# Kernel tuning notes

Hardware: AMD Instinct MI355X
Metric: run time of the kernel (lower is better)

The kernel has to match this reference:

```python
import jax, jax.numpy as jnp
import numpy as np

IN_C, HID1, HID2 = 128, 256, 32
N_NODES = 50000
N_EDGES = 1600000
N_LABEL = 200000


def setup_inputs() -> dict:
    key = jax.random.key(0)
    ks = jax.random.split(key, 8)
    x = jax.random.normal(ks[0], (N_NODES, IN_C), dtype=jnp.float32)
    edge_index = jax.random.randint(ks[1], (2, N_EDGES), 0, N_NODES, dtype=jnp.int64)
    edge_label_index = jax.random.randint(ks[2], (2, N_LABEL), 0, N_NODES, dtype=jnp.int64)
    # GCNConv params (glorot-ish scale), bias zeros as default init
    W1 = jax.random.normal(ks[3], (IN_C, HID1), dtype=jnp.float32) * (1.0 / np.sqrt(IN_C))
    b1 = jnp.zeros((HID1,), dtype=jnp.float32)
    W2 = jax.random.normal(ks[4], (HID1, HID2), dtype=jnp.float32) * (1.0 / np.sqrt(HID1))
    b2 = jnp.zeros((HID2,), dtype=jnp.float32)
    return {"x": x, "edge_index": edge_index, "edge_label_index": edge_label_index,
            "W1": W1, "b1": b1, "W2": W2, "b2": b2}


def _gcn_conv(x, W, b, src, dst, n_nodes):
    # GCNConv: h = x @ W; add self-loops; symmetric deg^{-1/2} normalization; scatter-add; + bias
    h = x @ W  # [N, out]
    loop = jnp.arange(n_nodes, dtype=src.dtype)
    s = jnp.concatenate([src, loop])
    d = jnp.concatenate([dst, loop])
    deg = jax.ops.segment_sum(jnp.ones_like(d, dtype=h.dtype), d, num_segments=n_nodes)
    dinv = jnp.where(deg > 0, jax.lax.rsqrt(deg), 0.0)
    coef = dinv[s] * dinv[d]  # [E+N]
    msg = h[s] * coef[:, None]  # irregular gather, [E+N, out]
    agg = jax.ops.segment_sum(msg, d, num_segments=n_nodes)
    return agg + b


def reference(x, edge_index, edge_label_index, W1, b1, W2, b2):
    n = x.shape[0]
    src, dst = edge_index[0], edge_index[1]
    # encode (dropout p=0, use_bn=False -> identity)
    h = _gcn_conv(x, W1, b1, src, dst, n)
    h = jax.nn.relu(h)
    z = _gcn_conv(h, W2, b2, src, dst, n)
    # decode: edge-wise dot product
    return (z[edge_label_index[0]] * z[edge_label_index[1]]).sum(axis=-1)
```

## Files before the change

kernel.cpp:

```cpp
#include <hip/hip_runtime.h>
#include <hip/hip_fp16.h>

#define IN_C 128
#define H1   256
#define H2   32
#define BWL  6
#define NBMAX 1024
#define BCAP 2560
#define CSRCAP 4096

typedef _Float16 half8 __attribute__((ext_vector_type(8)));
typedef _Float16 half4 __attribute__((ext_vector_type(4)));
typedef _Float16 h2    __attribute__((ext_vector_type(2)));
typedef float f32x4 __attribute__((ext_vector_type(4)));
typedef unsigned short us8 __attribute__((ext_vector_type(8)));
typedef unsigned short us4 __attribute__((ext_vector_type(4)));

__global__ __launch_bounds__(256) void k_scatter(const int* __restrict__ src, const int* __restrict__ dst,
                                                 int* bucket_cursor, unsigned int* __restrict__ binned,
                                                 const float* __restrict__ W1, const float* __restrict__ W2,
                                                 _Float16* __restrict__ W1s, _Float16* __restrict__ W2s,
                                                 int e, int nb) {
  __shared__ int hist[NBMAX];
  __shared__ int wbase[NBMAX];
  int t = threadIdx.x;
  for (int u = t; u < nb; u += 256) hist[u] = 0;
  __syncthreads();
  int base = blockIdx.x * 8192;
  int s_[32], d_[32], r_[32];
  #pragma unroll
  for (int j = 0; j < 32; j++) {
    int i = base + j * 256 + t;
    if (i < e) {
      s_[j] = src[i]; d_[j] = dst[i];
      r_[j] = atomicAdd(&hist[d_[j] >> BWL], 1);
    } else d_[j] = -1;
  }
  __syncthreads();
  for (int u = t; u < nb; u += 256) {
    int c = hist[u];
    wbase[u] = (c > 0) ? (u * BCAP + atomicAdd(&bucket_cursor[u], c)) : 0;
  }
  __syncthreads();
  #pragma unroll
  for (int j = 0; j < 32; j++) {
    if (d_[j] >= 0)
      binned[wbase[d_[j] >> BWL] + r_[j]] = ((unsigned)(d_[j] & 63) << 16) | (unsigned)s_[j];
  }
  int i = blockIdx.x * 256 + t;
  if (i < 128 * 256) {
    int d = i >> 3, j = i & 7;
    int mrow = d & 15, quad = (d >> 4) & 3, ks = (d >> 6) & 3, nt = d >> 8;
    W1s[i] = (_Float16)W1[(ks * 32 + quad * 8 + j) * 256 + nt * 16 + mrow];
  }
  if (i < 32 * 256) {
    int d = i >> 3, j = i & 7;
    int mrow = d & 15, quad = (d >> 4) & 3, ks = (d >> 6) & 7, nt = d >> 9;
    W2s[i] = (_Float16)W2[(ks * 32 + quad * 8 + j) * 32 + nt * 16 + mrow];
  }
}

__global__ __launch_bounds__(256) void k_fill2(const unsigned int* __restrict__ binned,
                                               const int* __restrict__ bucket_cursor,
                                               unsigned short* __restrict__ csr16,
                                               int* __restrict__ offsets, int* __restrict__ ecnt,
                                               float* __restrict__ dinv,
                                               const float4* __restrict__ x4, half4* __restrict__ xh4,
                                               int n, int nb) {
  __shared__ int cnt[64], pre[64], loc[64];
  __shared__ float sdinv[64];
  int b = blockIdx.x;
  int t = threadIdx.x;
  if (t < 64) cnt[t] = 0;
  {
    us8 dv;
    #pragma unroll
    for (int q = 0; q < 8; q++) dv[q] = (unsigned short)n;
    us8* cp = (us8*)(csr16 + (size_t)b * CSRCAP);
    for (int i = t; i < CSRCAP / 8; i += 256) cp[i] = dv;
  }
  __syncthreads();
  int start = b * BCAP, end = start + bucket_cursor[b];
  int startc = b * CSRCAP;
  int node0 = b << BWL;
  unsigned int recs[10]; int ranks[10];
  int ne = 0;
  for (int i = start + t; i < end; i += 256) {
    unsigned int rec = binned[i];
    int li = (int)(rec >> 16);
    ranks[ne] = atomicAdd(&cnt[li], 1);
    recs[ne++] = rec;
  }
  __syncthreads();
  int v = (t < 64) ? cnt[t] : 0;
  int vp = (v + 31) & ~31;
  if (t < 64) pre[t] = vp;
  __syncthreads();
  for (int off = 1; off < 64; off <<= 1) {
    int x = (t >= off && t < 64) ? pre[t - off] : 0;
    __syncthreads();
    if (t < 64) pre[t] += x;
    __syncthreads();
  }
  if (t < 64) {
    int excl = pre[t] - vp;
    loc[t] = excl;
    float dn = rsqrtf((float)(v + 1));
    sdinv[t] = dn;
    int node = node0 + t;
    if (node < n) {
      offsets[node] = startc + excl;
      ecnt[node] = v;
      dinv[node] = dn;
    }
  }
  __syncthreads();
  for (int k = 0; k < ne; k++) {
    int li = (int)(recs[k] >> 16);
    csr16[startc + loc[li] + ranks[k]] = (unsigned short)(recs[k] & 0xFFFFu);
  }
  for (int q = t; q < 64 * 32; q += 256) {
    int nd = node0 + (q >> 5);
    if (nd < n) {
      int c4 = q & 31;
      float4 vv = x4[(size_t)nd * 32 + c4];
      float dn = sdinv[q >> 5];
      half4 o;
      o[0] = (_Float16)(vv.x * dn); o[1] = (_Float16)(vv.y * dn);
      o[2] = (_Float16)(vv.z * dn); o[3] = (_Float16)(vv.w * dn);
      xh4[(size_t)nd * 32 + c4] = o;
    }
  }
}

__global__ __launch_bounds__(256) void k_agg1(const half8* __restrict__ xh8, const float* __restrict__ dinv,
                                              const int* __restrict__ ecnt, const int* __restrict__ offsets,
                                              const unsigned short* __restrict__ csr16,
                                              half8* __restrict__ aggh8, int n) {
  int node = blockIdx.x * 4 + (threadIdx.x >> 6);
  int lane = threadIdx.x & 63;
  int g = lane >> 4;
  int c8 = lane & 15;
  if (node >= n) return;
  float acc[8];
  #pragma unroll
  for (int k = 0; k < 8; k++) acc[k] = 0.f;
  int start = offsets[node];
  int cnt = ecnt[node];
  int units = ((cnt + 31) & ~31) >> 5;
  us8 idx = *(const us8*)(csr16 + start + g * 8);
  for (int u = 0; u < units; u++) {
    half8 v0 = xh8[(size_t)idx[0] * 16 + c8], v1 = xh8[(size_t)idx[1] * 16 + c8];
    half8 v2 = xh8[(size_t)idx[2] * 16 + c8], v3 = xh8[(size_t)idx[3] * 16 + c8];
    half8 v4 = xh8[(size_t)idx[4] * 16 + c8], v5 = xh8[(size_t)idx[5] * 16 + c8];
    half8 v6 = xh8[(size_t)idx[6] * 16 + c8], v7 = xh8[(size_t)idx[7] * 16 + c8];
    us8 nidx = *(const us8*)(csr16 + start + ((u + 1) << 5) + g * 8);
    asm volatile("" :: "v"(v0), "v"(v1), "v"(v2), "v"(v3), "v"(v4), "v"(v5), "v"(v6), "v"(v7));
    half8 s = (((v0 + v1) + (v2 + v3)) + ((v4 + v5) + (v6 + v7)));
    #pragma unroll
    for (int k = 0; k < 8; k++) acc[k] += (float)s[k];
    idx = nidx;
  }
  #pragma unroll
  for (int k = 0; k < 8; k++) {
    acc[k] += __shfl_xor(acc[k], 16, 64);
    acc[k] += __shfl_xor(acc[k], 32, 64);
  }
  if (g == 0) {
    half8 selfv = xh8[(size_t)node * 16 + c8];
    float dn = dinv[node];
    half8 o;
    #pragma unroll
    for (int k = 0; k < 8; k++) o[k] = (_Float16)((acc[k] + (float)selfv[k]) * dn);
    aggh8[(size_t)node * 16 + c8] = o;
  }
}

__global__ __launch_bounds__(256) void k_gemm12(const _Float16* __restrict__ aggh,
                                                const _Float16* __restrict__ W1s, const float* __restrict__ b1,
                                                const _Float16* __restrict__ W2s, const float* __restrict__ dinv,
                                                _Float16* __restrict__ h2h, int n) {
  __shared__ _Float16 wlds[128 * 256];
  int wid = threadIdx.x >> 6, lane = threadIdx.x & 63;
  int quad = lane >> 4, mrow = lane & 15;
  int mbase = blockIdx.x * 64 + wid * 16;
  int node = mbase + mrow; if (node >= n) node = n - 1;
  {
    half8* wl8 = (half8*)wlds;
    const half8* wg8 = (const half8*)W1s;
    for (int i = threadIdx.x; i < 4096; i += 256) wl8[i] = wg8[i];
  }
  __syncthreads();
  const half8* A = (const half8*)aggh;
  const half8* BL = (const half8*)wlds;
  f32x4 acc[16];
  #pragma unroll
  for (int t = 0; t < 16; t++) acc[t] = (f32x4){0.f, 0.f, 0.f, 0.f};
  half8 a_cur = A[(size_t)node * 16 + quad];
  #pragma unroll
  for (int ks = 0; ks < 4; ks++) {
    half8 a = a_cur;
    if (ks < 3) a_cur = A[(size_t)node * 16 + (ks + 1) * 4 + quad];
    #pragma unroll
    for (int nt = 0; nt < 16; nt++) {
      half8 b = BL[(nt * 4 + ks) * 64 + lane];
      acc[nt] = __builtin_amdgcn_mfma_f32_16x16x32_f16(a, b, acc[nt], 0, 0, 0);
    }
  }
  __syncthreads();
  _Float16* h1t = wlds;
  #pragma unroll
  for (int nt = 0; nt < 16; nt++) {
    int c = nt * 16 + mrow;
    float bias = b1[c];
    #pragma unroll
    for (int r = 0; r < 4; r++)
      h1t[(wid * 16 + quad * 4 + r) * 264 + c] = (_Float16)fmaxf(acc[nt][r] + bias, 0.f);
  }
  __syncthreads();
  const half8* B2 = (const half8*)W2s;
  f32x4 acc2[2];
  acc2[0] = (f32x4){0.f, 0.f, 0.f, 0.f};
  acc2[1] = (f32x4){0.f, 0.f, 0.f, 0.f};
  #pragma unroll
  for (int ks = 0; ks < 8; ks++) {
    const half8* arow = (const half8*)&h1t[(wid * 16 + mrow) * 264 + ks * 32 + quad * 8];
    half8 a = *arow;
    half8 b0 = B2[(0 * 8 + ks) * 64 + lane];
    half8 b1f = B2[(1 * 8 + ks) * 64 + lane];
    acc2[0] = __builtin_amdgcn_mfma_f32_16x16x32_f16(a, b0,  acc2[0], 0, 0, 0);
    acc2[1] = __builtin_amdgcn_mfma_f32_16x16x32_f16(a, b1f, acc2[1], 0, 0, 0);
  }
  #pragma unroll
  for (int nt = 0; nt < 2; nt++) {
    int c = nt * 16 + mrow;
    #pragma unroll
    for (int r = 0; r < 4; r++) {
      int m = mbase + quad * 4 + r;
      if (m < n) h2h[(size_t)m * H2 + c] = (_Float16)(acc2[nt][r] * dinv[m]);
    }
  }
}

__global__ __launch_bounds__(256) void k_agg2(const half4* __restrict__ h2h4, const float* __restrict__ dinv,
                                              const int* __restrict__ ecnt, const int* __restrict__ offsets,
                                              const unsigned short* __restrict__ csr16,
                                              const float* __restrict__ b2, half4* __restrict__ zh4, int n) {
  int node = blockIdx.x * 4 + (threadIdx.x >> 6);
  int lane = threadIdx.x & 63;
  int g = lane >> 3;
  int c4 = lane & 7;
  if (node >= n) return;
  float acc[4];
  #pragma unroll
  for (int k = 0; k < 4; k++) acc[k] = 0.f;
  int start = offsets[node];
  int cnt = ecnt[node];
  int units = ((cnt + 31) & ~31) >> 5;
  us4 idx = *(const us4*)(csr16 + start + g * 4);
  for (int u = 0; u < units; u++) {
    half4 vA = h2h4[(size_t)idx[0] * 8 + c4], vB = h2h4[(size_t)idx[1] * 8 + c4];
    half4 vC = h2h4[(size_t)idx[2] * 8 + c4], vD = h2h4[(size_t)idx[3] * 8 + c4];
    us4 nidx = *(const us4*)(csr16 + start + ((u + 1) << 5) + g * 4);
    asm volatile("" :: "v"(vA), "v"(vB), "v"(vC), "v"(vD));
    half4 sS = (vA + vB) + (vC + vD);
    #pragma unroll
    for (int k = 0; k < 4; k++) acc[k] += (float)sS[k];
    idx = nidx;
  }
  #pragma unroll
  for (int k = 0; k < 4; k++) {
    acc[k] += __shfl_xor(acc[k], 8, 64);
    acc[k] += __shfl_xor(acc[k], 16, 64);
    acc[k] += __shfl_xor(acc[k], 32, 64);
  }
  if (g == 0) {
    half4 selfv = h2h4[(size_t)node * 8 + c4];
    float dn = dinv[node];
    half4 o;
    #pragma unroll
    for (int k = 0; k < 4; k++) o[k] = (_Float16)((acc[k] + (float)selfv[k]) * dn + b2[c4 * 4 + k]);
    zh4[(size_t)node * 8 + c4] = o;
  }
}

__global__ __launch_bounds__(512) void k_decode(const half4* __restrict__ zh4, const int* __restrict__ eli,
                                                float* __restrict__ out, int L) {
  int p = blockIdx.x * 64 + (threadIdx.x >> 3);
  int c4 = threadIdx.x & 7;
  if (p >= L) return;
  int a = eli[p], b = eli[L + p];
  half4 za = zh4[(size_t)a * 8 + c4];
  half4 zb = zh4[(size_t)b * 8 + c4];
  h2 zal = {za[0], za[1]}, zah = {za[2], za[3]};
  h2 zbl = {zb[0], zb[1]}, zbh = {zb[2], zb[3]};
  float v = __builtin_amdgcn_fdot2(zal, zbl, __builtin_amdgcn_fdot2(zah, zbh, 0.f, false), false);
  #pragma unroll
  for (int off = 4; off >= 1; off >>= 1) v += __shfl_xor(v, off, 64);
  if (c4 == 0) out[p] = v;
}

extern "C" void kernel_launch(void* const* d_in, const int* in_sizes, int n_in,
                              void* d_out, int out_size, void* d_ws, size_t ws_size,
                              hipStream_t stream) {
  const float* x   = (const float*)d_in[0];
  const int*   ei  = (const int*)d_in[1];
  const int*   eli = (const int*)d_in[2];
  const float* W1  = (const float*)d_in[3];
  const float* b1  = (const float*)d_in[4];
  const float* W2  = (const float*)d_in[5];
  const float* b2  = (const float*)d_in[6];
  float* out = (float*)d_out;

  const int N = in_sizes[0] / IN_C;
  const int E = in_sizes[1] / 2;
  const int L = in_sizes[2] / 2;
  const int* e_src = ei;
  const int* e_dst = ei + E;
  const int NB = (N + 63) >> BWL;

  char* p = (char*)d_ws;
  auto carve = [&](size_t bytes) -> void* {
    void* r = (void*)p;
    p += (bytes + 255) & ~(size_t)255;
    return r;
  };
  int*   ecnt      = (int*)  carve((size_t)N * 4);
  float* dinv      = (float*)carve((size_t)N * 4);
  int*   offsets   = (int*)  carve((size_t)N * 4);
  int*   bcursor   = (int*)  carve((NBMAX + 1) * 4);
  _Float16* W1s    = (_Float16*)carve(256 * 128 * 2);
  _Float16* W2s    = (_Float16*)carve(32 * 256 * 2);
  unsigned short* csr16 = (unsigned short*)carve(((size_t)NB * CSRCAP + 64) * 2);
  unsigned int* binned  = (unsigned int*)carve((size_t)NB * BCAP * 4);
  h2*    xh        = (h2*)   carve((size_t)(N + 1) * IN_C * 2);
  h2*    aggh      = (h2*)   carve(((size_t)N + 64) * IN_C * 2);
  _Float16* h2h    = (_Float16*)carve(((size_t)N + 64) * H2 * 2);
  half4* zh4       = (half4*)carve((size_t)N * H2 * 2);
  half4* h2h4 = (half4*)h2h;

  const int B = 256;
  hipMemsetAsync(bcursor, 0, (size_t)(NBMAX + 1) * 4, stream);
  hipMemsetAsync((char*)xh + (size_t)N * IN_C * 2, 0, IN_C * 2, stream);
  hipMemsetAsync((char*)h2h + (size_t)N * H2 * 2, 0, H2 * 2, stream);
  k_scatter<<<(E + 8191) / 8192, B, 0, stream>>>(e_src, e_dst, bcursor, binned,
                                                 W1, W2, W1s, W2s, E, NB);
  k_fill2<<<NB, B, 0, stream>>>(binned, bcursor, csr16, offsets, ecnt, dinv,
                                (const float4*)x, (half4*)xh, N, NB);
  k_agg1<<<(N + 3) / 4, B, 0, stream>>>((const half8*)xh, dinv, ecnt, offsets, csr16, (half8*)aggh, N);
  k_gemm12<<<(N + 63) / 64, B, 0, stream>>>((const _Float16*)aggh, W1s, b1, W2s, dinv, h2h, N);
  k_agg2<<<(N + 3) / 4, B, 0, stream>>>(h2h4, dinv, ecnt, offsets, csr16, b2, zh4, N);
  k_decode<<<(L + 63) / 64, 512, 0, stream>>>(zh4, eli, out, L);
}
```

Measured before the change: 222.8 us.

## Pad CSR rows to 8 and restructure aggregation loops; fold dummy-row memsets into scatter

```diff
diff --git a/kernel.cpp b/kernel.cpp
--- a/kernel.cpp
+++ b/kernel.cpp
@@ -14,16 +14,20 @@
 typedef _Float16 h2    __attribute__((ext_vector_type(2)));
 typedef float f32x4 __attribute__((ext_vector_type(4)));
 typedef unsigned short us8 __attribute__((ext_vector_type(8)));
-typedef unsigned short us4 __attribute__((ext_vector_type(4)));
 
 __global__ __launch_bounds__(256) void k_scatter(const int* __restrict__ src, const int* __restrict__ dst,
                                                  int* bucket_cursor, unsigned int* __restrict__ binned,
                                                  const float* __restrict__ W1, const float* __restrict__ W2,
                                                  _Float16* __restrict__ W1s, _Float16* __restrict__ W2s,
+                                                 float* __restrict__ xh_dummy, float* __restrict__ h2h_dummy,
                                                  int e, int nb) {
   __shared__ int hist[NBMAX];
   __shared__ int wbase[NBMAX];
   int t = threadIdx.x;
+  if (blockIdx.x == 0) {
+    if (t < 64) xh_dummy[t] = 0.f;
+    if (t >= 64 && t < 80) h2h_dummy[t - 64] = 0.f;
+  }
   for (int u = t; u < nb; u += 256) hist[u] = 0;
   __syncthreads();
   int base = blockIdx.x * 8192;
@@ -93,7 +97,7 @@
   }
   __syncthreads();
   int v = (t < 64) ? cnt[t] : 0;
-  int vp = (v + 31) & ~31;
+  int vp = (v + 7) & ~7;
   if (t < 64) pre[t] = vp;
   __syncthreads();
   for (int off = 1; off < 64; off <<= 1) {
@@ -147,19 +151,17 @@
   for (int k = 0; k < 8; k++) acc[k] = 0.f;
   int start = offsets[node];
   int cnt = ecnt[node];
-  int units = ((cnt + 31) & ~31) >> 5;
-  us8 idx = *(const us8*)(csr16 + start + g * 8);
-  for (int u = 0; u < units; u++) {
-    half8 v0 = xh8[(size_t)idx[0] * 16 + c8], v1 = xh8[(size_t)idx[1] * 16 + c8];
-    half8 v2 = xh8[(size_t)idx[2] * 16 + c8], v3 = xh8[(size_t)idx[3] * 16 + c8];
-    half8 v4 = xh8[(size_t)idx[4] * 16 + c8], v5 = xh8[(size_t)idx[5] * 16 + c8];
-    half8 v6 = xh8[(size_t)idx[6] * 16 + c8], v7 = xh8[(size_t)idx[7] * 16 + c8];
-    us8 nidx = *(const us8*)(csr16 + start + ((u + 1) << 5) + g * 8);
-    asm volatile("" :: "v"(v0), "v"(v1), "v"(v2), "v"(v3), "v"(v4), "v"(v5), "v"(v6), "v"(v7));
-    half8 s = (((v0 + v1) + (v2 + v3)) + ((v4 + v5) + (v6 + v7)));
+  int qs = (cnt + 7) >> 3;
+  us8 id = *(const us8*)(csr16 + start);
+  for (int q = 0; q < qs; q++) {
+    int i0 = id[g], i1 = id[4 + g];
+    half8 v0 = xh8[(size_t)i0 * 16 + c8];
+    half8 v1 = xh8[(size_t)i1 * 16 + c8];
+    us8 nid = *(const us8*)(csr16 + start + (q + 1) * 8);
+    half8 s = v0 + v1;
     #pragma unroll
     for (int k = 0; k < 8; k++) acc[k] += (float)s[k];
-    idx = nidx;
+    id = nid;
   }
   #pragma unroll
   for (int k = 0; k < 8; k++) {
@@ -256,17 +258,22 @@
   for (int k = 0; k < 4; k++) acc[k] = 0.f;
   int start = offsets[node];
   int cnt = ecnt[node];
-  int units = ((cnt + 31) & ~31) >> 5;
-  us4 idx = *(const us4*)(csr16 + start + g * 4);
-  for (int u = 0; u < units; u++) {
-    half4 vA = h2h4[(size_t)idx[0] * 8 + c4], vB = h2h4[(size_t)idx[1] * 8 + c4];
-    half4 vC = h2h4[(size_t)idx[2] * 8 + c4], vD = h2h4[(size_t)idx[3] * 8 + c4];
-    us4 nidx = *(const us4*)(csr16 + start + ((u + 1) << 5) + g * 4);
-    asm volatile("" :: "v"(vA), "v"(vB), "v"(vC), "v"(vD));
-    half4 sS = (vA + vB) + (vC + vD);
-    #pragma unroll
-    for (int k = 0; k < 4; k++) acc[k] += (float)sS[k];
-    idx = nidx;
+  int qs = (cnt + 7) >> 3;
+  us8 id = *(const us8*)(csr16 + start);
+  for (int q = 0; q < qs; q += 2) {
+    us8 id2 = *(const us8*)(csr16 + start + (q + 1) * 8);
+    half4 v0 = h2h4[(size_t)(int)id[g] * 8 + c4];
+    half4 s;
+    if (q + 1 < qs) {
+      half4 v1 = h2h4[(size_t)(int)id2[g] * 8 + c4];
+      s = v0 + v1;
+    } else {
+      s = v0;
+    }
+    us8 nid = *(const us8*)(csr16 + start + (q + 2) * 8);
+    #pragma unroll
+    for (int k = 0; k < 4; k++) acc[k] += (float)s[k];
+    id = nid;
   }
   #pragma unroll
   for (int k = 0; k < 4; k++) {
@@ -341,10 +348,11 @@
 
   const int B = 256;
   hipMemsetAsync(bcursor, 0, (size_t)(NBMAX + 1) * 4, stream);
-  hipMemsetAsync((char*)xh + (size_t)N * IN_C * 2, 0, IN_C * 2, stream);
-  hipMemsetAsync((char*)h2h + (size_t)N * H2 * 2, 0, H2 * 2, stream);
   k_scatter<<<(E + 8191) / 8192, B, 0, stream>>>(e_src, e_dst, bcursor, binned,
-                                                 W1, W2, W1s, W2s, E, NB);
+                                                 W1, W2, W1s, W2s,
+                                                 (float*)((char*)xh + (size_t)N * IN_C * 2),
+                                                 (float*)((char*)h2h + (size_t)N * H2 * 2),
+                                                 E, NB);
   k_fill2<<<NB, B, 0, stream>>>(binned, bcursor, csr16, offsets, ecnt, dinv,
                                 (const float4*)x, (half4*)xh, N, NB);
   k_agg1<<<(N + 3) / 4, B, 0, stream>>>((const half8*)xh, dinv, ecnt, offsets, csr16, (half8*)aggh, N);
```

New measurement: 227.5 us. 2.1% more time.

## Replace two-pass bucketed CSR build with fixed-stride per-node atomic adjacency

Applied to the files above, without the earlier changes.

```diff
diff --git a/kernel.cpp b/kernel.cpp
--- a/kernel.cpp
+++ b/kernel.cpp
@@ -4,10 +4,7 @@
 #define IN_C 128
 #define H1   256
 #define H2   32
-#define BWL  6
-#define NBMAX 1024
-#define BCAP 2560
-#define CSRCAP 4096
+#define CSTRIDE 128
 
 typedef _Float16 half8 __attribute__((ext_vector_type(8)));
 typedef _Float16 half4 __attribute__((ext_vector_type(4)));
@@ -17,35 +14,25 @@
 typedef unsigned short us4 __attribute__((ext_vector_type(4)));
 
 __global__ __launch_bounds__(256) void k_scatter(const int* __restrict__ src, const int* __restrict__ dst,
-                                                 int* bucket_cursor, unsigned int* __restrict__ binned,
+                                                 int* __restrict__ ecnt, unsigned short* __restrict__ csr16,
                                                  const float* __restrict__ W1, const float* __restrict__ W2,
                                                  _Float16* __restrict__ W1s, _Float16* __restrict__ W2s,
-                                                 int e, int nb) {
-  __shared__ int hist[NBMAX];
-  __shared__ int wbase[NBMAX];
+                                                 float* __restrict__ xh_dummy, float* __restrict__ h2h_dummy,
+                                                 int e) {
   int t = threadIdx.x;
-  for (int u = t; u < nb; u += 256) hist[u] = 0;
-  __syncthreads();
+  if (blockIdx.x == 0) {
+    if (t < 64) xh_dummy[t] = 0.f;
+    if (t >= 64 && t < 80) h2h_dummy[t - 64] = 0.f;
+  }
   int base = blockIdx.x * 8192;
-  int s_[32], d_[32], r_[32];
   #pragma unroll
   for (int j = 0; j < 32; j++) {
     int i = base + j * 256 + t;
     if (i < e) {
-      s_[j] = src[i]; d_[j] = dst[i];
-      r_[j] = atomicAdd(&hist[d_[j] >> BWL], 1);
-    } else d_[j] = -1;
-  }
-  __syncthreads();
-  for (int u = t; u < nb; u += 256) {
-    int c = hist[u];
-    wbase[u] = (c > 0) ? (u * BCAP + atomicAdd(&bucket_cursor[u], c)) : 0;
-  }
-  __syncthreads();
-  #pragma unroll
-  for (int j = 0; j < 32; j++) {
-    if (d_[j] >= 0)
-      binned[wbase[d_[j] >> BWL] + r_[j]] = ((unsigned)(d_[j] & 63) << 16) | (unsigned)s_[j];
+      int s = src[i], d = dst[i];
+      int r = atomicAdd(&ecnt[d], 1);
+      csr16[(size_t)d * CSTRIDE + r] = (unsigned short)s;
+    }
   }
   int i = blockIdx.x * 256 + t;
   if (i < 128 * 256) {
@@ -60,65 +47,27 @@
   }
 }
 
-__global__ __launch_bounds__(256) void k_fill2(const unsigned int* __restrict__ binned,
-                                               const int* __restrict__ bucket_cursor,
-                                               unsigned short* __restrict__ csr16,
-                                               int* __restrict__ offsets, int* __restrict__ ecnt,
-                                               float* __restrict__ dinv,
-                                               const float4* __restrict__ x4, half4* __restrict__ xh4,
-                                               int n, int nb) {
-  __shared__ int cnt[64], pre[64], loc[64];
+__global__ __launch_bounds__(256) void k_fill(const int* __restrict__ ecnt, float* __restrict__ dinv,
+                                              unsigned short* __restrict__ csr16,
+                                              const float4* __restrict__ x4, half4* __restrict__ xh4,
+                                              int n) {
   __shared__ float sdinv[64];
   int b = blockIdx.x;
   int t = threadIdx.x;
-  if (t < 64) cnt[t] = 0;
-  {
-    us8 dv;
-    #pragma unroll
-    for (int q = 0; q < 8; q++) dv[q] = (unsigned short)n;
-    us8* cp = (us8*)(csr16 + (size_t)b * CSRCAP);
-    for (int i = t; i < CSRCAP / 8; i += 256) cp[i] = dv;
-  }
-  __syncthreads();
-  int start = b * BCAP, end = start + bucket_cursor[b];
-  int startc = b * CSRCAP;
-  int node0 = b << BWL;
-  unsigned int recs[10]; int ranks[10];
-  int ne = 0;
-  for (int i = start + t; i < end; i += 256) {
-    unsigned int rec = binned[i];
-    int li = (int)(rec >> 16);
-    ranks[ne] = atomicAdd(&cnt[li], 1);
-    recs[ne++] = rec;
-  }
-  __syncthreads();
-  int v = (t < 64) ? cnt[t] : 0;
-  int vp = (v + 31) & ~31;
-  if (t < 64) pre[t] = vp;
-  __syncthreads();
-  for (int off = 1; off < 64; off <<= 1) {
-    int x = (t >= off && t < 64) ? pre[t - off] : 0;
-    __syncthreads();
-    if (t < 64) pre[t] += x;
-    __syncthreads();
-  }
+  int node0 = b << 6;
   if (t < 64) {
-    int excl = pre[t] - vp;
-    loc[t] = excl;
-    float dn = rsqrtf((float)(v + 1));
-    sdinv[t] = dn;
     int node = node0 + t;
     if (node < n) {
-      offsets[node] = startc + excl;
-      ecnt[node] = v;
+      int v = ecnt[node];
+      float dn = rsqrtf((float)(v + 1));
       dinv[node] = dn;
-    }
-  }
-  __syncthreads();
-  for (int k = 0; k < ne; k++) {
-    int li = (int)(recs[k] >> 16);
-    csr16[startc + loc[li] + ranks[k]] = (unsigned short)(recs[k] & 0xFFFFu);
-  }
+      sdinv[t] = dn;
+      int vp = (v + 31) & ~31;
+      unsigned short* c = csr16 + (size_t)node * CSTRIDE;
+      for (int k = v; k < vp; k++) c[k] = (unsigned short)n;
+    }
+  }
+  __syncthreads();
   for (int q = t; q < 64 * 32; q += 256) {
     int nd = node0 + (q >> 5);
     if (nd < n) {
@@ -134,7 +83,7 @@
 }
 
 __global__ __launch_bounds__(256) void k_agg1(const half8* __restrict__ xh8, const float* __restrict__ dinv,
-                                              const int* __restrict__ ecnt, const int* __restrict__ offsets,
+                                              const int* __restrict__ ecnt,
                                               const unsigned short* __restrict__ csr16,
                                               half8* __restrict__ aggh8, int n) {
   int node = blockIdx.x * 4 + (threadIdx.x >> 6);
@@ -145,7 +94,7 @@
   float acc[8];
   #pragma unroll
   for (int k = 0; k < 8; k++) acc[k] = 0.f;
-  int start = offsets[node];
+  int start = node * CSTRIDE;
   int cnt = ecnt[node];
   int units = ((cnt + 31) & ~31) >> 5;
   us8 idx = *(const us8*)(csr16 + start + g * 8);
@@ -155,7 +104,6 @@
     half8 v4 = xh8[(size_t)idx[4] * 16 + c8], v5 = xh8[(size_t)idx[5] * 16 + c8];
     half8 v6 = xh8[(size_t)idx[6] * 16 + c8], v7 = xh8[(size_t)idx[7] * 16 + c8];
     us8 nidx = *(const us8*)(csr16 + start + ((u + 1) << 5) + g * 8);
-    asm volatile("" :: "v"(v0), "v"(v1), "v"(v2), "v"(v3), "v"(v4), "v"(v5), "v"(v6), "v"(v7));
     half8 s = (((v0 + v1) + (v2 + v3)) + ((v4 + v5) + (v6 + v7)));
     #pragma unroll
     for (int k = 0; k < 8; k++) acc[k] += (float)s[k];
@@ -243,7 +191,7 @@
 }
 
 __global__ __launch_bounds__(256) void k_agg2(const half4* __restrict__ h2h4, const float* __restrict__ dinv,
-                                              const int* __restrict__ ecnt, const int* __restrict__ offsets,
+                                              const int* __restrict__ ecnt,
                                               const unsigned short* __restrict__ csr16,
                                               const float* __restrict__ b2, half4* __restrict__ zh4, int n) {
   int node = blockIdx.x * 4 + (threadIdx.x >> 6);
@@ -254,7 +202,7 @@
   float acc[4];
   #pragma unroll
   for (int k = 0; k < 4; k++) acc[k] = 0.f;
-  int start = offsets[node];
+  int start = node * CSTRIDE;
   int cnt = ecnt[node];
   int units = ((cnt + 31) & ~31) >> 5;
   us4 idx = *(const us4*)(csr16 + start + g * 4);
@@ -262,7 +210,6 @@
     half4 vA = h2h4[(size_t)idx[0] * 8 + c4], vB = h2h4[(size_t)idx[1] * 8 + c4];
     half4 vC = h2h4[(size_t)idx[2] * 8 + c4], vD = h2h4[(size_t)idx[3] * 8 + c4];
     us4 nidx = *(const us4*)(csr16 + start + ((u + 1) << 5) + g * 4);
-    asm volatile("" :: "v"(vA), "v"(vB), "v"(vC), "v"(vD));
     half4 sS = (vA + vB) + (vC + vD);
     #pragma unroll
     for (int k = 0; k < 4; k++) acc[k] += (float)sS[k];
@@ -317,7 +264,7 @@
   const int L = in_sizes[2] / 2;
   const int* e_src = ei;
   const int* e_dst = ei + E;
-  const int NB = (N + 63) >> BWL;
+  const int NB = (N + 63) >> 6;
 
   char* p = (char*)d_ws;
   auto carve = [&](size_t bytes) -> void* {
@@ -327,12 +274,9 @@
   };
   int*   ecnt      = (int*)  carve((size_t)N * 4);
   float* dinv      = (float*)carve((size_t)N * 4);
-  int*   offsets   = (int*)  carve((size_t)N * 4);
-  int*   bcursor   = (int*)  carve((NBMAX + 1) * 4);
   _Float16* W1s    = (_Float16*)carve(256 * 128 * 2);
   _Float16* W2s    = (_Float16*)carve(32 * 256 * 2);
-  unsigned short* csr16 = (unsigned short*)carve(((size_t)NB * CSRCAP + 64) * 2);
-  unsigned int* binned  = (unsigned int*)carve((size_t)NB * BCAP * 4);
+  unsigned short* csr16 = (unsigned short*)carve(((size_t)N * CSTRIDE + 64) * 2);
   h2*    xh        = (h2*)   carve((size_t)(N + 1) * IN_C * 2);
   h2*    aggh      = (h2*)   carve(((size_t)N + 64) * IN_C * 2);
   _Float16* h2h    = (_Float16*)carve(((size_t)N + 64) * H2 * 2);
@@ -340,15 +284,15 @@
   half4* h2h4 = (half4*)h2h;
 
   const int B = 256;
-  hipMemsetAsync(bcursor, 0, (size_t)(NBMAX + 1) * 4, stream);
-  hipMemsetAsync((char*)xh + (size_t)N * IN_C * 2, 0, IN_C * 2, stream);
-  hipMemsetAsync((char*)h2h + (size_t)N * H2 * 2, 0, H2 * 2, stream);
-  k_scatter<<<(E + 8191) / 8192, B, 0, stream>>>(e_src, e_dst, bcursor, binned,
-                                                 W1, W2, W1s, W2s, E, NB);
-  k_fill2<<<NB, B, 0, stream>>>(binned, bcursor, csr16, offsets, ecnt, dinv,
-                                (const float4*)x, (half4*)xh, N, NB);
-  k_agg1<<<(N + 3) / 4, B, 0, stream>>>((const half8*)xh, dinv, ecnt, offsets, csr16, (half8*)aggh, N);
+  hipMemsetAsync(ecnt, 0, (size_t)N * 4, stream);
+  k_scatter<<<(E + 8191) / 8192, B, 0, stream>>>(e_src, e_dst, ecnt, csr16,
+                                                 W1, W2, W1s, W2s,
+                                                 (float*)((char*)xh + (size_t)N * IN_C * 2),
+                                                 (float*)((char*)h2h + (size_t)N * H2 * 2),
+                                                 E);
+  k_fill<<<NB, B, 0, stream>>>(ecnt, dinv, csr16, (const float4*)x, (half4*)xh, N);
+  k_agg1<<<(N + 3) / 4, B, 0, stream>>>((const half8*)xh, dinv, ecnt, csr16, (half8*)aggh, N);
   k_gemm12<<<(N + 63) / 64, B, 0, stream>>>((const _Float16*)aggh, W1s, b1, W2s, dinv, h2h, N);
-  k_agg2<<<(N + 3) / 4, B, 0, stream>>>(h2h4, dinv, ecnt, offsets, csr16, b2, zh4, N);
+  k_agg2<<<(N + 3) / 4, B, 0, stream>>>(h2h4, dinv, ecnt, csr16, b2, zh4, N);
   k_decode<<<(L + 63) / 64, 512, 0, stream>>>(zh4, eli, out, L);
 }
```

Result: slower. 261.7 us (+17.5%).
